# Kernel tuning notes

Hardware: AMD Instinct MI355X
Metric: run time of the kernel (lower is better)

## Reference

```python
import jax, jax.numpy as jnp
import numpy as np

BATCH, N_IN, N_OUT, D = 32768, 256, 256, 8

def setup_inputs() -> dict:
    key = jax.random.key(0)
    k1, k2 = jax.random.split(key)
    noise_std = 1.0 / (N_IN * (D + 1))
    x = jax.random.normal(k1, (BATCH, N_IN), dtype=jnp.float32)
    c_basis = noise_std * jax.random.normal(k2, (N_OUT, N_IN, D + 1), dtype=jnp.float32)
    c_act = jnp.ones((N_OUT, N_IN), dtype=jnp.float32)
    return {"x": x, "c_basis": c_basis, "c_act": c_act}

def _cheby_basis(x, degree):
    # x: (batch, n_in) -> (batch, n_in, degree+1) Chebyshev T_k(tanh(x))
    t = jnp.tanh(x)
    polys = [jnp.ones_like(t), t]
    for _ in range(2, degree + 1):
        polys.append(2.0 * t * polys[-1] - polys[-2])
    return jnp.stack(polys[: degree + 1], axis=-1)

def reference(x, c_basis, c_act):
    batch = x.shape[0]
    n_out = c_basis.shape[0]
    degree = c_basis.shape[-1] - 1
    Ti = _cheby_basis(x, degree)                      # (batch, n_in, D+1)
    cheb = Ti.reshape(batch, -1)                      # (batch, n_in*(D+1))
    cheb_w = (c_basis * c_act[..., None]).reshape(n_out, -1)
    return jnp.matmul(cheb, cheb_w.T)                 # (batch, n_out)
```

## Files before the change

kernel.cpp:

```cpp
#include <hip/hip_runtime.h>
#include <hip/hip_bf16.h>

#define BATCH 32768
#define NIN   256
#define NOUT  256

typedef __attribute__((ext_vector_type(8))) short bf16x8;
typedef __attribute__((ext_vector_type(4))) float f32x4;
typedef __attribute__((ext_vector_type(2))) float f32x2;
typedef __attribute__((ext_vector_type(4))) unsigned int u32x4;

static __device__ __forceinline__ unsigned short bf16_rne(float f) {
  unsigned u = __float_as_uint(f);
  u += 0x7fffu + ((u >> 16) & 1u);
  return (unsigned short)(u >> 16);
}

static __device__ __forceinline__ float fast_tanh(float v) {
  float a = fabsf(v);
  float z = __expf(-2.0f * a);
  float r = (1.0f - z) * __builtin_amdgcn_rcpf(1.0f + z);
  return copysignf(r, v);
}

static __device__ __forceinline__ unsigned pack_pair(f32x2 v) {
  __hip_bfloat162 h2 = __float22bfloat162_rn(make_float2(v[0], v[1]));
  union { __hip_bfloat162 h; unsigned u; } cv;
  cv.h = h2;
  return cv.u;
}

static __device__ __forceinline__ void init_state(const f32x4 x0, const f32x4 x1,
                                                  f32x2* cur, f32x2* prev,
                                                  f32x2* t2) {
  #pragma unroll
  for (int p = 0; p < 4; ++p) {
    float va = (p < 2) ? x0[2 * p]     : x1[2 * p - 4];
    float vb = (p < 2) ? x0[2 * p + 1] : x1[2 * p - 3];
    float ta = fast_tanh(va);
    float tb = fast_tanh(vb);
    cur[p]  = (f32x2){ta, tb};
    t2[p]   = cur[p] + cur[p];
    prev[p] = (f32x2){1.0f, 1.0f};
  }
}

static __device__ __forceinline__ void pipeline_barrier() {
  __builtin_amdgcn_sched_barrier(0);
  asm volatile("s_waitcnt lgkmcnt(0)" ::: "memory");
  __builtin_amdgcn_s_barrier();
  __builtin_amdgcn_sched_barrier(0);
}

__global__ void cheby_prepack(const float* __restrict__ cb,
                              const float* __restrict__ ca,
                              unsigned short* __restrict__ Bp) {
  int tid = blockIdx.x * 256 + threadIdx.x;
  int j    = tid & 7;
  int col  = (tid >> 3) & 15;
  int kg   = (tid >> 7) & 3;
  int tile = (tid >> 9) & 15;
  int ic   = (tid >> 13) & 7;
  int dm   = tid >> 16;
  int i = ic * 32 + kg * 8 + j;
  int n = tile * 16 + col;
  float w = cb[n * (NIN * 9) + i * 9 + (dm + 1)] * ca[n * NIN + i];
  Bp[tid] = bf16_rne(w);
}

__global__ void cheby_bias(const float* __restrict__ cb,
                           const float* __restrict__ ca,
                           float* __restrict__ bias) {
  int n = blockIdx.x;
  int l = threadIdx.x;
  float s = 0.0f;
  #pragma unroll
  for (int k = 0; k < 4; ++k) {
    int i = l + k * 64;
    s += cb[n * (NIN * 9) + i * 9] * ca[n * NIN + i];
  }
  #pragma unroll
  for (int off = 32; off; off >>= 1) s += __shfl_down(s, off);
  if (l == 0) bias[n] = s;
}

__global__ __launch_bounds__(256, 2)
void cheby_mfma(const float* __restrict__ x,
                const unsigned short* __restrict__ Bp,
                const float* __restrict__ bias,
                float* __restrict__ out) {
  __shared__ unsigned short Asm[2][8][4][512];

  int tid  = threadIdx.x;
  int w    = tid >> 6;
  int lane = tid & 63;
  int row16 = lane & 15;
  int kg    = lane >> 4;

  int base_row = blockIdx.x * 64;
  int tile0    = w * 4;

  const float* xw = x + (size_t)(base_row + w * 16 + row16) * NIN + kg * 8;
  char* wbase = (char*)Asm + (w * 1024 + lane * 16);
  const char* abase   = (const char*)Asm + lane * 16;
  const char* bp_lane = (const char*)Bp + kg * 256 + row16 * 16;

  f32x4 acc[4][4];
  #pragma unroll
  for (int a = 0; a < 4; ++a)
    #pragma unroll
    for (int b = 0; b < 4; ++b) acc[a][b] = (f32x4)0.0f;

  f32x4 xa = *(const f32x4*)xw;
  f32x4 xb = *(const f32x4*)(xw + 4);
  {
    f32x2 cur[4], prev[4], t2[4];
    init_state(xa, xb, cur, prev, t2);
    #pragma unroll
    for (int d = 1; d <= 8; ++d) {
      u32x4 pk;
      #pragma unroll
      for (int p = 0; p < 4; ++p) pk[p] = pack_pair(cur[p]);
      *(u32x4*)(wbase + (d - 1) * 4096) = pk;
      if (d < 8) {
        #pragma unroll
        for (int p = 0; p < 4; ++p) {
          f32x2 nx = __builtin_elementwise_fma(t2[p], cur[p], -prev[p]);
          prev[p] = cur[p];
          cur[p]  = nx;
        }
      }
    }
  }
  xa = *(const f32x4*)(xw + 32);
  xb = *(const f32x4*)(xw + 36);
  pipeline_barrier();

  for (int ic = 0; ic < 7; ++ic) {
    int buf = ic & 1;
    f32x2 cur[4], prev[4], t2[4];
    init_state(xa, xb, cur, prev, t2);
    if (ic < 6) {
      xa = *(const f32x4*)(xw + (ic + 2) * 32);
      xb = *(const f32x4*)(xw + (ic + 2) * 32 + 4);
    }
    const char* ai  = abase + buf * 32768;
    char*       wp  = wbase + (buf ^ 1) * 32768;
    const char* bpi = bp_lane + (size_t)(ic * 16 + tile0) * 1024;

    #pragma unroll
    for (int d = 1; d <= 8; ++d) {
      bf16x8 af[4], bfr[4];
      #pragma unroll
      for (int mt = 0; mt < 4; ++mt)
        af[mt] = *(const bf16x8*)(ai + (d - 1) * 4096 + mt * 1024);
      #pragma unroll
      for (int nt = 0; nt < 4; ++nt)
        bfr[nt] = *(const bf16x8*)(bpi + (size_t)(d - 1) * 131072 + nt * 1024);
      u32x4 pk;
      #pragma unroll
      for (int p = 0; p < 4; ++p) pk[p] = pack_pair(cur[p]);
      *(u32x4*)(wp + (d - 1) * 4096) = pk;
      if (d < 8) {
        #pragma unroll
        for (int p = 0; p < 4; ++p) {
          f32x2 nx = __builtin_elementwise_fma(t2[p], cur[p], -prev[p]);
          prev[p] = cur[p];
          cur[p]  = nx;
        }
      }
      __builtin_amdgcn_s_setprio(1);
      #pragma unroll
      for (int mt = 0; mt < 4; ++mt)
        #pragma unroll
        for (int nt = 0; nt < 4; ++nt)
          acc[mt][nt] = __builtin_amdgcn_mfma_f32_16x16x32_bf16(
              af[mt], bfr[nt], acc[mt][nt], 0, 0, 0);
      __builtin_amdgcn_s_setprio(0);
    }
    pipeline_barrier();
  }

  {
    const char* ai  = abase + 32768;
    const char* bpi = bp_lane + (size_t)(7 * 16 + tile0) * 1024;
    #pragma unroll
    for (int d = 1; d <= 8; ++d) {
      bf16x8 af[4], bfr[4];
      #pragma unroll
      for (int mt = 0; mt < 4; ++mt)
        af[mt] = *(const bf16x8*)(ai + (d - 1) * 4096 + mt * 1024);
      #pragma unroll
      for (int nt = 0; nt < 4; ++nt)
        bfr[nt] = *(const bf16x8*)(bpi + (size_t)(d - 1) * 131072 + nt * 1024);
      __builtin_amdgcn_s_setprio(1);
      #pragma unroll
      for (int mt = 0; mt < 4; ++mt)
        #pragma unroll
        for (int nt = 0; nt < 4; ++nt)
          acc[mt][nt] = __builtin_amdgcn_mfma_f32_16x16x32_bf16(
              af[mt], bfr[nt], acc[mt][nt], 0, 0, 0);
      __builtin_amdgcn_s_setprio(0);
    }
  }

  #pragma unroll
  for (int nt = 0; nt < 4; ++nt) {
    int c = (tile0 + nt) * 16 + row16;
    float bv = bias[c];
    #pragma unroll
    for (int mt = 0; mt < 4; ++mt) {
      int r0 = base_row + mt * 16 + kg * 4;
      #pragma unroll
      for (int q = 0; q < 4; ++q)
        out[(size_t)(r0 + q) * NOUT + c] = acc[mt][nt][q] + bv;
    }
  }
}

extern "C" void kernel_launch(void* const* d_in, const int* in_sizes, int n_in,
                              void* d_out, int out_size, void* d_ws, size_t ws_size,
                              hipStream_t stream) {
  const float* x  = (const float*)d_in[0];
  const float* cb = (const float*)d_in[1];
  const float* ca = (const float*)d_in[2];
  float* out = (float*)d_out;

  unsigned short* Bp = (unsigned short*)d_ws;
  float* bias = (float*)((char*)d_ws + 8 * NIN * NOUT * 2);

  cheby_prepack<<<(8 * NIN * NOUT) / 256, 256, 0, stream>>>(cb, ca, Bp);
  cheby_bias<<<NOUT, 64, 0, stream>>>(cb, ca, bias);
  cheby_mfma<<<512, 256, 0, stream>>>(x, Bp, bias, out);
}
```

Baseline: 50.36 us.

## Batch-prefetch all B fragments per chunk and double-buffer A LDS reads

Each chunk now issues all 32 global B-fragment loads up front, before the Chebyshev basis compute and LDS writes, so global latency overlaps that ALU work. The basis-generation loop is split from the MFMA loop by a sched barrier. A-fragment reads from LDS are software-pipelined one degree ahead of the MFMAs. This raises register pressure (128 extra VGPRs for B fragments) under launch_bounds(256,2), which risks spills or lower occupancy.

New measurement: 51.88 us. 1.03x slower.

```diff
diff --git a/kernel.cpp b/kernel.cpp
--- a/kernel.cpp
+++ b/kernel.cpp
@@ -138,25 +138,19 @@
 
   for (int ic = 0; ic < 7; ++ic) {
     int buf = ic & 1;
+    const char* bpi = bp_lane + (size_t)(ic * 16 + tile0) * 1024;
+    bf16x8 bfr[8][4];
+    #pragma unroll
+    for (int dd = 0; dd < 8; ++dd)
+      #pragma unroll
+      for (int nt = 0; nt < 4; ++nt)
+        bfr[dd][nt] = *(const bf16x8*)(bpi + (size_t)dd * 131072 + nt * 1024);
+
     f32x2 cur[4], prev[4], t2[4];
     init_state(xa, xb, cur, prev, t2);
-    if (ic < 6) {
-      xa = *(const f32x4*)(xw + (ic + 2) * 32);
-      xb = *(const f32x4*)(xw + (ic + 2) * 32 + 4);
-    }
-    const char* ai  = abase + buf * 32768;
-    char*       wp  = wbase + (buf ^ 1) * 32768;
-    const char* bpi = bp_lane + (size_t)(ic * 16 + tile0) * 1024;
-
+    char* wp = wbase + (buf ^ 1) * 32768;
     #pragma unroll
     for (int d = 1; d <= 8; ++d) {
-      bf16x8 af[4], bfr[4];
-      #pragma unroll
-      for (int mt = 0; mt < 4; ++mt)
-        af[mt] = *(const bf16x8*)(ai + (d - 1) * 4096 + mt * 1024);
-      #pragma unroll
-      for (int nt = 0; nt < 4; ++nt)
-        bfr[nt] = *(const bf16x8*)(bpi + (size_t)(d - 1) * 131072 + nt * 1024);
       u32x4 pk;
       #pragma unroll
       for (int p = 0; p < 4; ++p) pk[p] = pack_pair(cur[p]);
@@ -169,38 +163,75 @@
           cur[p]  = nx;
         }
       }
+    }
+    if (ic < 6) {
+      xa = *(const f32x4*)(xw + (ic + 2) * 32);
+      xb = *(const f32x4*)(xw + (ic + 2) * 32 + 4);
+    }
+    __builtin_amdgcn_sched_barrier(0);
+
+    const char* ai = abase + buf * 32768;
+    bf16x8 afc[4];
+    #pragma unroll
+    for (int mt = 0; mt < 4; ++mt)
+      afc[mt] = *(const bf16x8*)(ai + mt * 1024);
+    #pragma unroll
+    for (int d = 0; d < 8; ++d) {
+      bf16x8 afn[4];
+      if (d < 7) {
+        #pragma unroll
+        for (int mt = 0; mt < 4; ++mt)
+          afn[mt] = *(const bf16x8*)(ai + (d + 1) * 4096 + mt * 1024);
+      }
       __builtin_amdgcn_s_setprio(1);
       #pragma unroll
       for (int mt = 0; mt < 4; ++mt)
         #pragma unroll
         for (int nt = 0; nt < 4; ++nt)
           acc[mt][nt] = __builtin_amdgcn_mfma_f32_16x16x32_bf16(
-              af[mt], bfr[nt], acc[mt][nt], 0, 0, 0);
+              afc[mt], bfr[d][nt], acc[mt][nt], 0, 0, 0);
       __builtin_amdgcn_s_setprio(0);
+      if (d < 7) {
+        #pragma unroll
+        for (int mt = 0; mt < 4; ++mt) afc[mt] = afn[mt];
+      }
     }
     pipeline_barrier();
   }
 
   {
-    const char* ai  = abase + 32768;
     const char* bpi = bp_lane + (size_t)(7 * 16 + tile0) * 1024;
-    #pragma unroll
-    for (int d = 1; d <= 8; ++d) {
-      bf16x8 af[4], bfr[4];
-      #pragma unroll
-      for (int mt = 0; mt < 4; ++mt)
-        af[mt] = *(const bf16x8*)(ai + (d - 1) * 4096 + mt * 1024);
+    bf16x8 bfr[8][4];
+    #pragma unroll
+    for (int dd = 0; dd < 8; ++dd)
       #pragma unroll
       for (int nt = 0; nt < 4; ++nt)
-        bfr[nt] = *(const bf16x8*)(bpi + (size_t)(d - 1) * 131072 + nt * 1024);
+        bfr[dd][nt] = *(const bf16x8*)(bpi + (size_t)dd * 131072 + nt * 1024);
+    const char* ai = abase + 32768;
+    bf16x8 afc[4];
+    #pragma unroll
+    for (int mt = 0; mt < 4; ++mt)
+      afc[mt] = *(const bf16x8*)(ai + mt * 1024);
+    #pragma unroll
+    for (int d = 0; d < 8; ++d) {
+      bf16x8 afn[4];
+      if (d < 7) {
+        #pragma unroll
+        for (int mt = 0; mt < 4; ++mt)
+          afn[mt] = *(const bf16x8*)(ai + (d + 1) * 4096 + mt * 1024);
+      }
       __builtin_amdgcn_s_setprio(1);
       #pragma unroll
       for (int mt = 0; mt < 4; ++mt)
         #pragma unroll
         for (int nt = 0; nt < 4; ++nt)
           acc[mt][nt] = __builtin_amdgcn_mfma_f32_16x16x32_bf16(
-              af[mt], bfr[nt], acc[mt][nt], 0, 0, 0);
+              afc[mt], bfr[d][nt], acc[mt][nt], 0, 0, 0);
       __builtin_amdgcn_s_setprio(0);
+      if (d < 7) {
+        #pragma unroll
+        for (int mt = 0; mt < 4; ++mt) afc[mt] = afn[mt];
+      }
     }
   }
 
```

## Software-pipeline A/B fragment loads one step ahead with per-step barriers

Applied to the files above, without the earlier changes.

Restructures the main MFMA loop so A (LDS) and B (global) fragments for the next degree step load into double-buffered registers while the current step's MFMAs run. The next chunk's Chebyshev state is initialized inside the loop. The per-chunk barrier with an explicit lgkmcnt wait becomes a lightweight s_barrier at every inner step. This aims to hide load latency behind MFMA issue, but it adds eight barriers per chunk and more register pressure under a 2-blocks/SM launch bound. Correctness depends on the compiler inserting the needed waitcnts before LDS reuse across barriers.

New measurement: 47.76 us. 5.2% less time.

```diff
diff --git a/kernel.cpp b/kernel.cpp
--- a/kernel.cpp
+++ b/kernel.cpp
@@ -45,9 +45,8 @@
   }
 }
 
-static __device__ __forceinline__ void pipeline_barrier() {
-  __builtin_amdgcn_sched_barrier(0);
-  asm volatile("s_waitcnt lgkmcnt(0)" ::: "memory");
+static __device__ __forceinline__ void phase_barrier() {
+  __builtin_amdgcn_sched_barrier(0);
   __builtin_amdgcn_s_barrier();
   __builtin_amdgcn_sched_barrier(0);
 }
@@ -114,92 +113,129 @@
   f32x4 xa = *(const f32x4*)xw;
   f32x4 xb = *(const f32x4*)(xw + 4);
   {
-    f32x2 cur[4], prev[4], t2[4];
-    init_state(xa, xb, cur, prev, t2);
+    f32x2 c0[4], p0[4], t0[4];
+    init_state(xa, xb, c0, p0, t0);
     #pragma unroll
     for (int d = 1; d <= 8; ++d) {
       u32x4 pk;
       #pragma unroll
-      for (int p = 0; p < 4; ++p) pk[p] = pack_pair(cur[p]);
+      for (int q = 0; q < 4; ++q) pk[q] = pack_pair(c0[q]);
       *(u32x4*)(wbase + (d - 1) * 4096) = pk;
       if (d < 8) {
         #pragma unroll
-        for (int p = 0; p < 4; ++p) {
-          f32x2 nx = __builtin_elementwise_fma(t2[p], cur[p], -prev[p]);
-          prev[p] = cur[p];
-          cur[p]  = nx;
+        for (int q = 0; q < 4; ++q) {
+          f32x2 nx = __builtin_elementwise_fma(t0[q], c0[q], -p0[q]);
+          p0[q] = c0[q];
+          c0[q] = nx;
         }
       }
     }
   }
   xa = *(const f32x4*)(xw + 32);
   xb = *(const f32x4*)(xw + 36);
-  pipeline_barrier();
+  f32x2 cur[4], prev[4], t2[4];
+  init_state(xa, xb, cur, prev, t2);
+
+  bf16x8 af[2][4], bfr[2][4];
+  {
+    const char* bp0 = bp_lane + (size_t)tile0 * 1024;
+    #pragma unroll
+    for (int nt = 0; nt < 4; ++nt)
+      bfr[0][nt] = *(const bf16x8*)(bp0 + nt * 1024);
+  }
+  __builtin_amdgcn_sched_barrier(0);
+  asm volatile("s_waitcnt lgkmcnt(0)" ::: "memory");
+  __builtin_amdgcn_s_barrier();
+  __builtin_amdgcn_sched_barrier(0);
+  #pragma unroll
+  for (int mt = 0; mt < 4; ++mt)
+    af[0][mt] = *(const bf16x8*)(abase + mt * 1024);
 
   for (int ic = 0; ic < 7; ++ic) {
-    int buf = ic & 1;
-    f32x2 cur[4], prev[4], t2[4];
-    init_state(xa, xb, cur, prev, t2);
-    if (ic < 6) {
-      xa = *(const f32x4*)(xw + (ic + 2) * 32);
-      xb = *(const f32x4*)(xw + (ic + 2) * 32 + 4);
-    }
-    const char* ai  = abase + buf * 32768;
-    char*       wp  = wbase + (buf ^ 1) * 32768;
-    const char* bpi = bp_lane + (size_t)(ic * 16 + tile0) * 1024;
-
-    #pragma unroll
-    for (int d = 1; d <= 8; ++d) {
-      bf16x8 af[4], bfr[4];
+    const char* ai   = abase + (ic & 1) * 32768;
+    const char* ain  = abase + ((ic + 1) & 1) * 32768;
+    char*       wp   = wbase + ((ic + 1) & 1) * 32768;
+    const char* bpi  = bp_lane + (size_t)(ic * 16 + tile0) * 1024;
+    const char* bpin = bp_lane + (size_t)((ic + 1) * 16 + tile0) * 1024;
+
+    #pragma unroll
+    for (int p = 0; p < 8; ++p) {
+      if (p < 7) {
+        #pragma unroll
+        for (int mt = 0; mt < 4; ++mt)
+          af[(p + 1) & 1][mt] =
+              *(const bf16x8*)(ai + (p + 1) * 4096 + mt * 1024);
+      } else {
+        #pragma unroll
+        for (int mt = 0; mt < 4; ++mt)
+          af[0][mt] = *(const bf16x8*)(ain + mt * 1024);
+      }
+      if (p < 7) {
+        #pragma unroll
+        for (int nt = 0; nt < 4; ++nt)
+          bfr[(p + 1) & 1][nt] =
+              *(const bf16x8*)(bpi + (size_t)(p + 1) * 131072 + nt * 1024);
+      } else {
+        #pragma unroll
+        for (int nt = 0; nt < 4; ++nt)
+          bfr[0][nt] = *(const bf16x8*)(bpin + nt * 1024);
+      }
+      {
+        u32x4 pk;
+        #pragma unroll
+        for (int q = 0; q < 4; ++q) pk[q] = pack_pair(cur[q]);
+        *(u32x4*)(wp + p * 4096) = pk;
+        if (p < 7) {
+          #pragma unroll
+          for (int q = 0; q < 4; ++q) {
+            f32x2 nx = __builtin_elementwise_fma(t2[q], cur[q], -prev[q]);
+            prev[q] = cur[q];
+            cur[q]  = nx;
+          }
+        }
+      }
+      if (p == 3 && ic <= 5) {
+        xa = *(const f32x4*)(xw + (ic + 2) * 32);
+        xb = *(const f32x4*)(xw + (ic + 2) * 32 + 4);
+      }
+      if (p == 7 && ic <= 5)
+        init_state(xa, xb, cur, prev, t2);
+
+      phase_barrier();
+
+      __builtin_amdgcn_s_setprio(1);
       #pragma unroll
       for (int mt = 0; mt < 4; ++mt)
-        af[mt] = *(const bf16x8*)(ai + (d - 1) * 4096 + mt * 1024);
-      #pragma unroll
-      for (int nt = 0; nt < 4; ++nt)
-        bfr[nt] = *(const bf16x8*)(bpi + (size_t)(d - 1) * 131072 + nt * 1024);
-      u32x4 pk;
-      #pragma unroll
-      for (int p = 0; p < 4; ++p) pk[p] = pack_pair(cur[p]);
-      *(u32x4*)(wp + (d - 1) * 4096) = pk;
-      if (d < 8) {
-        #pragma unroll
-        for (int p = 0; p < 4; ++p) {
-          f32x2 nx = __builtin_elementwise_fma(t2[p], cur[p], -prev[p]);
-          prev[p] = cur[p];
-          cur[p]  = nx;
-        }
-      }
-      __builtin_amdgcn_s_setprio(1);
-      #pragma unroll
-      for (int mt = 0; mt < 4; ++mt)
         #pragma unroll
         for (int nt = 0; nt < 4; ++nt)
           acc[mt][nt] = __builtin_amdgcn_mfma_f32_16x16x32_bf16(
-              af[mt], bfr[nt], acc[mt][nt], 0, 0, 0);
+              af[p & 1][mt], bfr[p & 1][nt], acc[mt][nt], 0, 0, 0);
       __builtin_amdgcn_s_setprio(0);
     }
-    pipeline_barrier();
   }
 
   {
     const char* ai  = abase + 32768;
     const char* bpi = bp_lane + (size_t)(7 * 16 + tile0) * 1024;
     #pragma unroll
-    for (int d = 1; d <= 8; ++d) {
-      bf16x8 af[4], bfr[4];
+    for (int p = 0; p < 8; ++p) {
+      if (p < 7) {
+        #pragma unroll
+        for (int mt = 0; mt < 4; ++mt)
+          af[(p + 1) & 1][mt] =
+              *(const bf16x8*)(ai + (p + 1) * 4096 + mt * 1024);
+        #pragma unroll
+        for (int nt = 0; nt < 4; ++nt)
+          bfr[(p + 1) & 1][nt] =
+              *(const bf16x8*)(bpi + (size_t)(p + 1) * 131072 + nt * 1024);
+      }
+      __builtin_amdgcn_s_setprio(1);
       #pragma unroll
       for (int mt = 0; mt < 4; ++mt)
-        af[mt] = *(const bf16x8*)(ai + (d - 1) * 4096 + mt * 1024);
-      #pragma unroll
-      for (int nt = 0; nt < 4; ++nt)
-        bfr[nt] = *(const bf16x8*)(bpi + (size_t)(d - 1) * 131072 + nt * 1024);
-      __builtin_amdgcn_s_setprio(1);
-      #pragma unroll
-      for (int mt = 0; mt < 4; ++mt)
         #pragma unroll
         for (int nt = 0; nt < 4; ++nt)
           acc[mt][nt] = __builtin_amdgcn_mfma_f32_16x16x32_bf16(
-              af[mt], bfr[nt], acc[mt][nt], 0, 0, 0);
+              af[p & 1][mt], bfr[p & 1][nt], acc[mt][nt], 0, 0, 0);
       __builtin_amdgcn_s_setprio(0);
     }
   }
```
